# Performance work log

Hardware: AMD Instinct MI355X
Metric: run time of the kernel (lower is better)

## Reference

```python
import jax, jax.numpy as jnp
import numpy as np

N = 20000          # nodes
E = 320000         # edges (avg degree 16)
D_IN, D1, D2, D_OUT = 256, 512, 256, 64
EPS = 1e-5


def _glorot(key, shape):
    lim = (6.0 / (shape[0] + shape[1])) ** 0.5
    return jax.random.uniform(key, shape, jnp.float32, -lim, lim)


def setup_inputs() -> dict:
    key = jax.random.key(0)
    ks = jax.random.split(key, 8)
    x = jax.random.normal(ks[0], (N, D_IN), jnp.float32)
    edge_index = jax.random.randint(ks[1], (2, E), 0, N, dtype=jnp.int64)
    return {
        "x": x,
        "edge_index": edge_index,
        # SAGEConv 1 (SoftmaxAggregation temperature t1 over inp_dim channels)
        "t1": jnp.ones((1, D_IN), jnp.float32),
        "Wl1": _glorot(ks[2], (D_IN, D1)), "bl1": jnp.zeros((D1,), jnp.float32),
        "Wr1": _glorot(ks[3], (D_IN, D1)),
        "g1": jnp.ones((D1,), jnp.float32), "beta1": jnp.zeros((D1,), jnp.float32),
        # SAGEConv 2
        "t2": jnp.ones((1, D1), jnp.float32),
        "Wl2": _glorot(ks[4], (D1, D2)), "bl2": jnp.zeros((D2,), jnp.float32),
        "Wr2": _glorot(ks[5], (D1, D2)),
        "g2": jnp.ones((D2,), jnp.float32), "beta2": jnp.zeros((D2,), jnp.float32),
        # final linear + LayerNorm
        "Wf": _glorot(ks[6], (D2, D_OUT)), "bf": jnp.zeros((D_OUT,), jnp.float32),
        "gx": jnp.ones((D_OUT,), jnp.float32), "betax": jnp.zeros((D_OUT,), jnp.float32),
    }


def _sage_softmax(x, src, dst, t, Wl, bl, Wr, n):
    """SAGEConv with learnable per-channel SoftmaxAggregation."""
    m = x[src]                                              # [E, C] gathered messages
    a = m * t                                               # scaled logits
    amax = jax.ops.segment_max(a, dst, num_segments=n)      # [N, C]
    e = jnp.exp(a - amax[dst])
    denom = jax.ops.segment_sum(e, dst, num_segments=n)     # [N, C]
    w = e / denom[dst]                                      # segment softmax weights
    agg = jax.ops.segment_sum(m * w, dst, num_segments=n)   # weighted neighbor sum
    return agg @ Wl + bl + x @ Wr


def _graph_ln(x, g, b):
    # PyG LayerNorm mode='graph', batch=None: normalize over ALL nodes & channels
    mu = x.mean()
    std = jnp.sqrt(((x - mu) ** 2).mean())
    return (x - mu) / (std + EPS) * g + b


def _ln(x, g, b):
    mu = x.mean(-1, keepdims=True)
    var = ((x - mu) ** 2).mean(-1, keepdims=True)
    return (x - mu) / jnp.sqrt(var + EPS) * g + b


def reference(x, edge_index, t1, Wl1, bl1, Wr1, g1, beta1,
              t2, Wl2, bl2, Wr2, g2, beta2, Wf, bf, gx, betax):
    src, dst = edge_index[0], edge_index[1]
    h = _sage_softmax(x, src, dst, t1, Wl1, bl1, Wr1, N)
    h = jax.nn.relu(_graph_ln(h, g1, beta1))
    h = _sage_softmax(h, src, dst, t2, Wl2, bl2, Wr2, N)
    h = jax.nn.relu(_graph_ln(h, g2, beta2))
    p = h.mean(0, keepdims=True)                            # global_mean_pool, batch=None -> [1, 256]
    out = _ln(p @ Wf + bf, gx, betax)
    return jax.nn.relu(out)
```

## Files before the change

### kernel.cpp

```cpp
#include <hip/hip_runtime.h>
#include <math.h>

#define NODES 20000
#define MPAD  20096
#define EDGES 320000
#define EPSV  1e-5f
#define LOG2E 1.4426950408889634f

#define PREP_CNT   1250
#define PREP_CAST  5000
#define PREP_TR    512
#define PREP_TOTAL (PREP_CNT + PREP_CAST + PREP_TR + 1)

typedef short bf16x8 __attribute__((ext_vector_type(8)));
typedef float f32x4  __attribute__((ext_vector_type(4)));
typedef float f2     __attribute__((ext_vector_type(2)));

__device__ __forceinline__ unsigned short f2bf(float f) {
    unsigned int u = __float_as_uint(f);
    u = (u + 0x7fffu + ((u >> 16) & 1u)) >> 16;
    return (unsigned short)u;
}
__device__ __forceinline__ float bf2f(unsigned short h) {
    return __uint_as_float(((unsigned int)h) << 16);
}

__device__ __forceinline__ void load_lds16(const unsigned short* g, unsigned short* l) {
    __builtin_amdgcn_global_load_lds(
        (const __attribute__((address_space(1))) unsigned int*)g,
        (__attribute__((address_space(3))) unsigned int*)l, 16, 0, 0);
}

__global__ void k_prep(const int* __restrict__ dst, int* __restrict__ counts,
                       const float* __restrict__ x, unsigned short* __restrict__ xb,
                       const float* __restrict__ Wl1, const float* __restrict__ Wr1,
                       const float* __restrict__ Wl2, const float* __restrict__ Wr2,
                       unsigned short* __restrict__ o1l, unsigned short* __restrict__ o1r,
                       unsigned short* __restrict__ o2l, unsigned short* __restrict__ o2r,
                       float* __restrict__ acc, float* __restrict__ colsum) {
    int b = blockIdx.x;
    int t = threadIdx.x;
    if (b < PREP_CNT) {
        int e = b * 256 + t;
        if (e < EDGES) atomicAdd(&counts[dst[e]], 1);
    } else if (b < PREP_CNT + PREP_CAST) {
        int i = ((b - PREP_CNT) * 256 + t) * 4;
        float4 v = *(const float4*)(x + i);
        xb[i + 0] = f2bf(v.x); xb[i + 1] = f2bf(v.y);
        xb[i + 2] = f2bf(v.z); xb[i + 3] = f2bf(v.w);
    } else if (b < PREP_CNT + PREP_CAST + PREP_TR) {
        __shared__ float tile[32][33];
        int zz = b - PREP_CNT - PREP_CAST;
        int z = zz >> 7;
        int idx = zz & 127;
        const float* W = (z == 0) ? Wl1 : (z == 1) ? Wr1 : (z == 2) ? Wl2 : Wr2;
        unsigned short* Wt = (z == 0) ? o1l : (z == 1) ? o1r : (z == 2) ? o2l : o2r;
        int K = (z < 2) ? 256 : 512, N = (z < 2) ? 512 : 256;
        int nb = N / 32;
        int n0 = (idx % nb) * 32, k0 = (idx / nb) * 32;
        int tx = t & 31, ty = t >> 5;
#pragma unroll
        for (int j = 0; j < 4; j++)
            tile[ty + j * 8][tx] = W[(size_t)(k0 + ty + j * 8) * N + n0 + tx];
        __syncthreads();
#pragma unroll
        for (int j = 0; j < 4; j++)
            Wt[(size_t)(n0 + ty + j * 8) * K + k0 + tx] = f2bf(tile[tx][ty + j * 8]);
    } else {
        if (t < 4) acc[t] = 0.f;
        colsum[t] = 0.f;
    }
}

__global__ void k_scan(const int* __restrict__ counts, int* __restrict__ offs) {
    __shared__ int ssum[256];
    int t = threadIdx.x;
    const int chunk = (NODES + 255) / 256;
    int b = t * chunk, e = b + chunk;
    if (b > NODES) b = NODES;
    if (e > NODES) e = NODES;
    int s = 0;
    for (int i = b; i < e; i++) s += counts[i];
    ssum[t] = s;
    __syncthreads();
    int v = s;
#pragma unroll
    for (int o = 1; o < 256; o <<= 1) {
        int add = (t >= o) ? ssum[t - o] : 0;
        __syncthreads();
        v += add;
        ssum[t] = v;
        __syncthreads();
    }
    int run = v - s;
    if (t == 255) offs[NODES] = v;
    for (int i = b; i < e; i++) { offs[i] = run; run += counts[i]; }
}

__global__ void k_scatter(const int* __restrict__ src, const int* __restrict__ dst,
                          const int* __restrict__ offs, int* __restrict__ cursor,
                          int* __restrict__ csr_src) {
    int e = blockIdx.x * blockDim.x + threadIdx.x;
    if (e < EDGES) {
        int d = dst[e];
        int pos = atomicAdd(&cursor[d], 1);
        csr_src[offs[d] + pos] = src[e];
    }
}

template <int C, int S, int UNR>
__global__ void k_agg(const unsigned short* __restrict__ xb, const float* __restrict__ tt,
                      const int* __restrict__ offs, const int* __restrict__ csr,
                      unsigned short* __restrict__ out) {
    constexpr int CS  = C / S;
    constexpr int VPL = CS / 64;
    constexpr int W   = VPL / 2;
    typedef unsigned int uv __attribute__((ext_vector_type(W)));
    typedef unsigned short usv __attribute__((ext_vector_type(VPL)));
    int waveg = (int)((blockIdx.x * (unsigned)blockDim.x + threadIdx.x) >> 6);
    int lane = threadIdx.x & 63;
    int node = waveg / S;
    int slice = waveg % S;
    if (node >= NODES) return;
    int beg = __builtin_amdgcn_readfirstlane(offs[node]);
    int end = __builtin_amdgcn_readfirstlane(offs[node + 1]);
    int cb = slice * CS + lane * VPL;
    const unsigned short* __restrict__ xcb = xb + cb;
    f2 tl[W], l[W], s[W];
#pragma unroll
    for (int i = 0; i < W; i++) {
        tl[i][0] = tt[cb + 2 * i] * LOG2E;
        tl[i][1] = tt[cb + 2 * i + 1] * LOG2E;
        l[i][0] = 0.f; l[i][1] = 0.f;
        s[i][0] = 0.f; s[i][1] = 0.f;
    }
    int k = beg;
    for (; k + UNR <= end; k += UNR) {
        uv v[UNR];
#pragma unroll
        for (int u = 0; u < UNR; u++) {
            int sn = csr[k + u];
            v[u] = *(const uv*)(xcb + (size_t)sn * C);
        }
#pragma unroll
        for (int u = 0; u < UNR; u++)
#pragma unroll
            for (int i = 0; i < W; i++) {
                unsigned wd = v[u][i];
                f2 xv;
                xv[0] = __uint_as_float(wd << 16);
                xv[1] = __uint_as_float(wd & 0xffff0000u);
                f2 a = xv * tl[i];
                f2 p;
                p[0] = __builtin_amdgcn_exp2f(a[0]);
                p[1] = __builtin_amdgcn_exp2f(a[1]);
                l[i] += p;
                s[i] = __builtin_elementwise_fma(p, xv, s[i]);
            }
    }
    for (; k < end; k++) {
        int sn = csr[k];
        uv vv = *(const uv*)(xcb + (size_t)sn * C);
#pragma unroll
        for (int i = 0; i < W; i++) {
            unsigned wd = vv[i];
            f2 xv;
            xv[0] = __uint_as_float(wd << 16);
            xv[1] = __uint_as_float(wd & 0xffff0000u);
            f2 a = xv * tl[i];
            f2 p;
            p[0] = __builtin_amdgcn_exp2f(a[0]);
            p[1] = __builtin_amdgcn_exp2f(a[1]);
            l[i] += p;
            s[i] = __builtin_elementwise_fma(p, xv, s[i]);
        }
    }
    bool has = end > beg;
    usv o;
#pragma unroll
    for (int i = 0; i < W; i++) {
        o[2 * i]     = f2bf(has ? s[i][0] / l[i][0] : 0.f);
        o[2 * i + 1] = f2bf(has ? s[i][1] / l[i][1] : 0.f);
    }
    *(usv*)(out + (size_t)node * C + cb) = o;
}

template <int K, int NT>
__global__ __launch_bounds__(256) void k_gemm_mfma(
    const unsigned short* __restrict__ A1, const unsigned short* __restrict__ B1t,
    const unsigned short* __restrict__ A2, const unsigned short* __restrict__ B2t,
    const float* __restrict__ bias, unsigned short* __restrict__ Co, int M,
    float* __restrict__ stat) {
    __shared__ short As[128 * 32];
    __shared__ short Bs[128 * 32];
    __shared__ float rs[256], rq[256];

    int t = threadIdx.x;
    int m0 = blockIdx.x * 128, n0 = blockIdx.y * 128;
    int wv = t >> 6, lane = t & 63;
    int wm = wv & 1, wn = wv >> 1;
    int lm = lane & 15, quad = lane >> 4;
    int sr = t >> 2;
    int sc8 = (t & 3) * 8;

    f32x4 acc[4][4] = {};

    for (int ph = 0; ph < 2; ph++) {
        const unsigned short* __restrict__ A  = ph ? A2 : A1;
        const unsigned short* __restrict__ Bt = ph ? B2t : B1t;
        for (int k0 = 0; k0 < K; k0 += 32) {
#pragma unroll
            for (int it = 0; it < 2; it++) {
                load_lds16(A  + (size_t)(m0 + it * 64 + sr) * K + k0 + sc8,
                           (unsigned short*)&As[it * 2048 + wv * 512]);
                load_lds16(Bt + (size_t)(n0 + it * 64 + sr) * K + k0 + sc8,
                           (unsigned short*)&Bs[it * 2048 + wv * 512]);
            }
            __syncthreads();
            bf16x8 af[4], bfr[4];
#pragma unroll
            for (int i = 0; i < 4; i++) {
                af[i]  = *(const bf16x8*)&As[(wm * 64 + i * 16 + lm) * 32 + quad * 8];
                bfr[i] = *(const bf16x8*)&Bs[(wn * 64 + i * 16 + lm) * 32 + quad * 8];
            }
#pragma unroll
            for (int mi = 0; mi < 4; mi++)
#pragma unroll
                for (int nj = 0; nj < 4; nj++)
                    acc[mi][nj] = __builtin_amdgcn_mfma_f32_16x16x32_bf16(
                        af[mi], bfr[nj], acc[mi][nj], 0, 0, 0);
            __syncthreads();
        }
    }

    float sum = 0.f, ss = 0.f;
#pragma unroll
    for (int mi = 0; mi < 4; mi++) {
        int rb = m0 + wm * 64 + mi * 16 + quad * 4;
#pragma unroll
        for (int nj = 0; nj < 4; nj++) {
            int col = n0 + wn * 64 + nj * 16 + lm;
            float bb = bias[col];
#pragma unroll
            for (int rg = 0; rg < 4; rg++) {
                int row = rb + rg;
                if (row < M) {
                    float y = acc[mi][nj][rg] + bb;
                    Co[(size_t)row * NT + col] = f2bf(y);
                    sum += y; ss += y * y;
                }
            }
        }
    }
    rs[t] = sum; rq[t] = ss;
    __syncthreads();
    for (int o = 128; o > 0; o >>= 1) {
        if (t < o) { rs[t] += rs[t + o]; rq[t] += rq[t + o]; }
        __syncthreads();
    }
    if (t == 0) { atomicAdd(&stat[0], rs[0]); atomicAdd(&stat[1], rq[0]); }
}

template <int C>
__global__ void k_ln_relu_b(unsigned short* __restrict__ h, int n,
                            const float* __restrict__ st,
                            const float* __restrict__ g, const float* __restrict__ b) {
    typedef unsigned short us8 __attribute__((ext_vector_type(8)));
    float mu = st[0] / (float)n;
    float var = st[1] / (float)n - mu * mu;
    var = var < 0.f ? 0.f : var;
    float inv = 1.0f / (sqrtf(var) + EPSV);
    int i8 = (blockIdx.x * blockDim.x + threadIdx.x) * 8;
    if (i8 >= n) return;
    int c = i8 & (C - 1);
    us8 v = *(const us8*)(h + i8);
    us8 o;
#pragma unroll
    for (int j = 0; j < 8; j++) {
        float y = (bf2f(v[j]) - mu) * inv * g[c + j] + b[c + j];
        o[j] = f2bf(fmaxf(y, 0.f));
    }
    *(us8*)(h + i8) = o;
}

__global__ void k_ln_colsum(const unsigned short* __restrict__ h, int n,
                            const float* __restrict__ st,
                            const float* __restrict__ g, const float* __restrict__ b,
                            float* __restrict__ colsum) {
    float mu = st[0] / (float)n;
    float var = st[1] / (float)n - mu * mu;
    var = var < 0.f ? 0.f : var;
    float inv = 1.0f / (sqrtf(var) + EPSV);
    int t = threadIdx.x;
    float gv = g[t], bv = b[t];
    float local = 0.f;
    int stride = gridDim.x * blockDim.x;
    for (int i = blockIdx.x * blockDim.x + t; i < n; i += stride) {
        float y = (bf2f(h[i]) - mu) * inv * gv + bv;
        local += fmaxf(y, 0.f);
    }
    atomicAdd(&colsum[t], local);
}

__global__ void k_final(const float* __restrict__ colsum, const float* __restrict__ Wf,
                        const float* __restrict__ bf, const float* __restrict__ gx,
                        const float* __restrict__ bx, float* __restrict__ out) {
    __shared__ float p[256];
    int t = threadIdx.x;
    p[t] = colsum[t] * (1.0f / (float)NODES);
    __syncthreads();
    if (t < 64) {
        float acc = bf[t];
        for (int c = 0; c < 256; c++) acc = fmaf(p[c], Wf[c * 64 + t], acc);
        float sum = acc;
        for (int o = 32; o > 0; o >>= 1) sum += __shfl_xor(sum, o);
        float mu = sum * (1.0f / 64.0f);
        float d = acc - mu;
        float vs = d * d;
        for (int o = 32; o > 0; o >>= 1) vs += __shfl_xor(vs, o);
        float var = vs * (1.0f / 64.0f);
        float y = d * rsqrtf(var + EPSV) * gx[t] + bx[t];
        out[t] = fmaxf(y, 0.f);
    }
}

extern "C" void kernel_launch(void* const* d_in, const int* in_sizes, int n_in,
                              void* d_out, int out_size, void* d_ws, size_t ws_size,
                              hipStream_t stream) {
    const float* x   = (const float*)d_in[0];
    const int*   ei  = (const int*)d_in[1];
    const float* t1  = (const float*)d_in[2];
    const float* Wl1 = (const float*)d_in[3];
    const float* bl1 = (const float*)d_in[4];
    const float* Wr1 = (const float*)d_in[5];
    const float* g1  = (const float*)d_in[6];
    const float* be1 = (const float*)d_in[7];
    const float* t2  = (const float*)d_in[8];
    const float* Wl2 = (const float*)d_in[9];
    const float* bl2 = (const float*)d_in[10];
    const float* Wr2 = (const float*)d_in[11];
    const float* g2  = (const float*)d_in[12];
    const float* be2 = (const float*)d_in[13];
    const float* Wf  = (const float*)d_in[14];
    const float* bf  = (const float*)d_in[15];
    const float* gx  = (const float*)d_in[16];
    const float* bx  = (const float*)d_in[17];
    float* out = (float*)d_out;

    char* ws = (char*)d_ws;
    size_t off = 0;
    auto alloc = [&](size_t bytes) { size_t o = off; off = (off + bytes + 511) & ~511ull; return o; };
    size_t o_counts = alloc((size_t)NODES * 4);
    size_t o_cursor = alloc((size_t)NODES * 4);
    size_t zero_bytes = off;
    size_t o_acc    = alloc(4 * 4);
    size_t o_colsum = alloc(256 * 4);
    size_t o_offs = alloc((size_t)(NODES + 1) * 4);
    size_t o_csrc = alloc((size_t)EDGES * 4);
    size_t o_w1l  = alloc((size_t)512 * 256 * 2);
    size_t o_w1r  = alloc((size_t)512 * 256 * 2);
    size_t o_w2l  = alloc((size_t)256 * 512 * 2);
    size_t o_w2r  = alloc((size_t)256 * 512 * 2);
    size_t o_bufX = alloc((size_t)MPAD * 256 * 2);
    size_t o_agg  = alloc((size_t)MPAD * 512 * 2);
    size_t o_h1   = alloc((size_t)MPAD * 512 * 2);

    int*   counts = (int*)(ws + o_counts);
    int*   cursor = (int*)(ws + o_cursor);
    float* acc    = (float*)(ws + o_acc);
    float* colsum = (float*)(ws + o_colsum);
    int*   offs   = (int*)(ws + o_offs);
    int*   csrc   = (int*)(ws + o_csrc);
    unsigned short* w1lt = (unsigned short*)(ws + o_w1l);
    unsigned short* w1rt = (unsigned short*)(ws + o_w1r);
    unsigned short* w2lt = (unsigned short*)(ws + o_w2l);
    unsigned short* w2rt = (unsigned short*)(ws + o_w2r);
    unsigned short* xb   = (unsigned short*)(ws + o_bufX);
    unsigned short* h2p  = (unsigned short*)(ws + o_bufX);
    unsigned short* aggb = (unsigned short*)(ws + o_agg);
    unsigned short* h1   = (unsigned short*)(ws + o_h1);

    const int* src = ei;
    const int* dst = ei + EDGES;

    hipMemsetAsync(ws, 0, zero_bytes, stream);

    k_prep<<<PREP_TOTAL, 256, 0, stream>>>(dst, counts, x, xb,
                                           Wl1, Wr1, Wl2, Wr2,
                                           w1lt, w1rt, w2lt, w2rt,
                                           acc, colsum);
    k_scan<<<1, 256, 0, stream>>>(counts, offs);
    k_scatter<<<(EDGES + 255) / 256, 256, 0, stream>>>(src, dst, offs, cursor, csrc);

    k_agg<256, 2, 8><<<(NODES * 2 + 3) / 4, 256, 0, stream>>>(xb, t1, offs, csrc, aggb);
    k_gemm_mfma<256, 512><<<dim3(MPAD / 128, 4), 256, 0, stream>>>(
        aggb, w1lt, xb, w1rt, bl1, h1, NODES, acc);
    k_ln_relu_b<512><<<NODES * 512 / 8 / 256, 256, 0, stream>>>(h1, NODES * 512, acc, g1, be1);

    k_agg<512, 2, 4><<<(NODES * 2 + 3) / 4, 256, 0, stream>>>(h1, t2, offs, csrc, aggb);
    k_gemm_mfma<512, 256><<<dim3(MPAD / 128, 2), 256, 0, stream>>>(
        aggb, w2lt, h1, w2rt, bl2, h2p, NODES, acc + 2);

    k_ln_colsum<<<1024, 256, 0, stream>>>(h2p, NODES * 256, acc + 2, g2, be2, colsum);
    k_final<<<1, 256, 0, stream>>>(colsum, Wf, bf, gx, bx, out);
}
```

Baseline: 349.2 us.

## Use one channel per lane in softmax aggregation with channel-slice blocks

Rewrites the neighbor softmax-aggregation kernel so each lane handles a single bf16 channel and each block covers four nodes for one 64-channel slice. This replaces the earlier scheme of two slices per node with each lane loading a vector of channels. The aim is more waves in flight and a deeper per-lane unroll to hide gather latency. In exchange, each gather becomes a 2-byte scalar load, so there are more memory instructions per byte moved, and the S-fold slice split raises the number of csr/offs reads.

```diff
diff --git a/kernel.cpp b/kernel.cpp
--- a/kernel.cpp
+++ b/kernel.cpp
@@ -14,7 +14,6 @@
 
 typedef short bf16x8 __attribute__((ext_vector_type(8)));
 typedef float f32x4  __attribute__((ext_vector_type(4)));
-typedef float f2     __attribute__((ext_vector_type(2)));
 
 __device__ __forceinline__ unsigned short f2bf(float f) {
     unsigned int u = __float_as_uint(f);
@@ -109,80 +108,44 @@
 }
 
 template <int C, int S, int UNR>
-__global__ void k_agg(const unsigned short* __restrict__ xb, const float* __restrict__ tt,
-                      const int* __restrict__ offs, const int* __restrict__ csr,
-                      unsigned short* __restrict__ out) {
-    constexpr int CS  = C / S;
-    constexpr int VPL = CS / 64;
-    constexpr int W   = VPL / 2;
-    typedef unsigned int uv __attribute__((ext_vector_type(W)));
-    typedef unsigned short usv __attribute__((ext_vector_type(VPL)));
-    int waveg = (int)((blockIdx.x * (unsigned)blockDim.x + threadIdx.x) >> 6);
-    int lane = threadIdx.x & 63;
-    int node = waveg / S;
-    int slice = waveg % S;
+__global__ void k_agg_s(const unsigned short* __restrict__ xb, const float* __restrict__ tt,
+                        const int* __restrict__ offs, const int* __restrict__ csr,
+                        unsigned short* __restrict__ out) {
+    static_assert(C / S == 64, "one channel per lane");
+    int t = threadIdx.x;
+    int lane = t & 63;
+    int slice = blockIdx.x % S;
+    int node = (blockIdx.x / S) * 4 + (t >> 6);
     if (node >= NODES) return;
     int beg = __builtin_amdgcn_readfirstlane(offs[node]);
     int end = __builtin_amdgcn_readfirstlane(offs[node + 1]);
-    int cb = slice * CS + lane * VPL;
-    const unsigned short* __restrict__ xcb = xb + cb;
-    f2 tl[W], l[W], s[W];
-#pragma unroll
-    for (int i = 0; i < W; i++) {
-        tl[i][0] = tt[cb + 2 * i] * LOG2E;
-        tl[i][1] = tt[cb + 2 * i + 1] * LOG2E;
-        l[i][0] = 0.f; l[i][1] = 0.f;
-        s[i][0] = 0.f; s[i][1] = 0.f;
-    }
+    int c = slice * 64 + lane;
+    const unsigned short* __restrict__ xc = xb + c;
+    float tl = tt[c] * LOG2E;
+    float l = 0.f, s = 0.f;
     int k = beg;
     for (; k + UNR <= end; k += UNR) {
-        uv v[UNR];
+        float xv[UNR];
 #pragma unroll
         for (int u = 0; u < UNR; u++) {
             int sn = csr[k + u];
-            v[u] = *(const uv*)(xcb + (size_t)sn * C);
+            xv[u] = bf2f(xc[(size_t)sn * C]);
         }
 #pragma unroll
-        for (int u = 0; u < UNR; u++)
-#pragma unroll
-            for (int i = 0; i < W; i++) {
-                unsigned wd = v[u][i];
-                f2 xv;
-                xv[0] = __uint_as_float(wd << 16);
-                xv[1] = __uint_as_float(wd & 0xffff0000u);
-                f2 a = xv * tl[i];
-                f2 p;
-                p[0] = __builtin_amdgcn_exp2f(a[0]);
-                p[1] = __builtin_amdgcn_exp2f(a[1]);
-                l[i] += p;
-                s[i] = __builtin_elementwise_fma(p, xv, s[i]);
-            }
+        for (int u = 0; u < UNR; u++) {
+            float p = __builtin_amdgcn_exp2f(xv[u] * tl);
+            l += p;
+            s = fmaf(p, xv[u], s);
+        }
     }
     for (; k < end; k++) {
         int sn = csr[k];
-        uv vv = *(const uv*)(xcb + (size_t)sn * C);
-#pragma unroll
-        for (int i = 0; i < W; i++) {
-            unsigned wd = vv[i];
-            f2 xv;
-            xv[0] = __uint_as_float(wd << 16);
-            xv[1] = __uint_as_float(wd & 0xffff0000u);
-            f2 a = xv * tl[i];
-            f2 p;
-            p[0] = __builtin_amdgcn_exp2f(a[0]);
-            p[1] = __builtin_amdgcn_exp2f(a[1]);
-            l[i] += p;
-            s[i] = __builtin_elementwise_fma(p, xv, s[i]);
-        }
-    }
-    bool has = end > beg;
-    usv o;
-#pragma unroll
-    for (int i = 0; i < W; i++) {
-        o[2 * i]     = f2bf(has ? s[i][0] / l[i][0] : 0.f);
-        o[2 * i + 1] = f2bf(has ? s[i][1] / l[i][1] : 0.f);
-    }
-    *(usv*)(out + (size_t)node * C + cb) = o;
+        float xv = bf2f(xc[(size_t)sn * C]);
+        float p = __builtin_amdgcn_exp2f(xv * tl);
+        l += p;
+        s = fmaf(p, xv, s);
+    }
+    out[(size_t)node * C + c] = f2bf(end > beg ? s / l : 0.f);
 }
 
 template <int K, int NT>
@@ -392,12 +355,12 @@
     k_scan<<<1, 256, 0, stream>>>(counts, offs);
     k_scatter<<<(EDGES + 255) / 256, 256, 0, stream>>>(src, dst, offs, cursor, csrc);
 
-    k_agg<256, 2, 8><<<(NODES * 2 + 3) / 4, 256, 0, stream>>>(xb, t1, offs, csrc, aggb);
+    k_agg_s<256, 4, 8><<<(NODES / 4) * 4, 256, 0, stream>>>(xb, t1, offs, csrc, aggb);
     k_gemm_mfma<256, 512><<<dim3(MPAD / 128, 4), 256, 0, stream>>>(
         aggb, w1lt, xb, w1rt, bl1, h1, NODES, acc);
     k_ln_relu_b<512><<<NODES * 512 / 8 / 256, 256, 0, stream>>>(h1, NODES * 512, acc, g1, be1);
 
-    k_agg<512, 2, 4><<<(NODES * 2 + 3) / 4, 256, 0, stream>>>(h1, t2, offs, csrc, aggb);
+    k_agg_s<512, 8, 8><<<(NODES / 4) * 8, 256, 0, stream>>>(h1, t2, offs, csrc, aggb);
     k_gemm_mfma<512, 256><<<dim3(MPAD / 128, 2), 256, 0, stream>>>(
         aggb, w2lt, h1, w2rt, bl2, h2p, NODES, acc + 2);
 
```

Measured after the change: 371.5 us. 6.4% more time.
